# Optimization experiments

Measured on AMD Instinct MI355X. Metric: run time of the kernel, lower is better.

The kernel has to match this reference:

```python
import jax, jax.numpy as jnp
import numpy as np

NEG_BIG = -9e15

def setup_inputs() -> dict:
    key = jax.random.key(0)
    k1, k2, k3, k4 = jax.random.split(key, 4)
    N, Fin, Fout = 8192, 256, 128
    x = jax.random.normal(k1, (N, Fin), dtype=jnp.float32)
    adj = jax.random.randint(k2, (N, N), 0, 2, dtype=jnp.int32)
    # xavier-uniform-like init
    limW = float(np.sqrt(6.0 / (Fin + Fout)))
    W = jax.random.uniform(k3, (Fin, Fout), minval=-limW, maxval=limW, dtype=jnp.float32)
    lima = float(np.sqrt(6.0 / (2 * Fout + 1)))
    a = jax.random.uniform(k4, (2 * Fout, 1), minval=-lima, maxval=lima, dtype=jnp.float32)
    return {"x": x, "adj": adj, "W": W, "a": a}

def reference(x, adj, W, a, alpha=0.2):
    # h: (N, Fout)
    h = x @ W
    Fout = W.shape[1]
    # Split a into source/target halves: e[i,j] = leakyrelu(h_i·a1 + h_j·a2)
    a1, a2 = a[:Fout, 0], a[Fout:, 0]
    s = h @ a1  # (N,) row (source) scores
    t = h @ a2  # (N,) col (target) scores
    e = jax.nn.leaky_relu(s[:, None] + t[None, :], negative_slope=alpha)  # (N, N)
    e = jnp.where(adj > 0, e, NEG_BIG)
    attention = jax.nn.softmax(e, axis=1)
    # dropout omitted (eval mode / training=False)
    return attention @ h
```

## Files before the change

kernel.cpp:

```cpp
#include <hip/hip_runtime.h>
#include <hip/hip_bf16.h>

typedef __attribute__((ext_vector_type(8))) short short8;
typedef __attribute__((ext_vector_type(4))) short short4v;
typedef __attribute__((ext_vector_type(4))) float f32x4;

#define NR 8192
#define LOG2E 1.4426950408889634f

__device__ __forceinline__ short f2bf(float f) {
  return __builtin_bit_cast(short, __float2bfloat16(f));
}

__global__ __launch_bounds__(256) void k_pack(const int* __restrict__ adj,
                                              unsigned* __restrict__ mask) {
  size_t gid = (size_t)blockIdx.x * 256 + threadIdx.x;
  const int4* p = (const int4*)&adj[gid * 32];
  unsigned m = 0;
#pragma unroll
  for (int c = 0; c < 8; ++c) {
    int4 v = p[c];
    m |= (unsigned)(v.x > 0) << (c * 4 + 0);
    m |= (unsigned)(v.y > 0) << (c * 4 + 1);
    m |= (unsigned)(v.z > 0) << (c * 4 + 2);
    m |= (unsigned)(v.w > 0) << (c * 4 + 3);
  }
  mask[gid] = m;
}

__global__ __launch_bounds__(256) void k_gemm_h(const float* __restrict__ x,
                                                const float* __restrict__ W,
                                                const float* __restrict__ a,
                                                short* __restrict__ HT2,
                                                float* __restrict__ sv,
                                                float* __restrict__ tv) {
  __shared__ short WT[128][136];
  const int tid = threadIdx.x;
  const int w = tid >> 6;
  const int L = tid & 63;
  const int lm = L & 15;
  const int q = L >> 4;
  const int i0 = blockIdx.x * 64;

  f32x4 acc[8];
#pragma unroll
  for (int nn = 0; nn < 8; ++nn) acc[nn] = (f32x4){0.f, 0.f, 0.f, 0.f};

  for (int kc = 0; kc < 256; kc += 128) {
    if (kc) __syncthreads();
#pragma unroll
    for (int p = 0; p < 16; ++p) {
      int idx = p * 256 + tid;
      int k = idx >> 5;
      int f4 = (idx & 31) * 4;
      float4 v = *(const float4*)&W[(kc + k) * 128 + f4];
      WT[f4 + 0][k] = f2bf(v.x);
      WT[f4 + 1][k] = f2bf(v.y);
      WT[f4 + 2][k] = f2bf(v.z);
      WT[f4 + 3][k] = f2bf(v.w);
    }
    __syncthreads();
#pragma unroll
    for (int ks = 0; ks < 4; ++ks) {
      int row = i0 + 16 * w + lm;
      const float* xp = &x[(size_t)row * 256 + kc + ks * 32 + q * 8];
      float4 xa = *(const float4*)xp;
      float4 xb = *(const float4*)(xp + 4);
      short8 af;
      af[0] = f2bf(xa.x); af[1] = f2bf(xa.y); af[2] = f2bf(xa.z); af[3] = f2bf(xa.w);
      af[4] = f2bf(xb.x); af[5] = f2bf(xb.y); af[6] = f2bf(xb.z); af[7] = f2bf(xb.w);
#pragma unroll
      for (int nn = 0; nn < 8; ++nn) {
        short8 bf = *(const short8*)&WT[nn * 16 + lm][ks * 32 + q * 8];
        acc[nn] = __builtin_amdgcn_mfma_f32_16x16x32_bf16(af, bf, acc[nn], 0, 0, 0);
      }
    }
  }

  const int ib = i0 + 16 * w + 4 * q;
  const int tbase = (ib >> 5) * 4096 + (ib & 31);
  float a1v[8], a2v[8];
#pragma unroll
  for (int nn = 0; nn < 8; ++nn) {
    a1v[nn] = a[nn * 16 + lm];
    a2v[nn] = a[128 + nn * 16 + lm];
  }
  float sr[4] = {0.f, 0.f, 0.f, 0.f};
  float tr[4] = {0.f, 0.f, 0.f, 0.f};
#pragma unroll
  for (int nn = 0; nn < 8; ++nn) {
    int f = nn * 16 + lm;
    short4v o;
    o[0] = f2bf(acc[nn][0]);
    o[1] = f2bf(acc[nn][1]);
    o[2] = f2bf(acc[nn][2]);
    o[3] = f2bf(acc[nn][3]);
    *(short4v*)&HT2[tbase + f * 32] = o;
#pragma unroll
    for (int r = 0; r < 4; ++r) {
      sr[r] += acc[nn][r] * a1v[nn];
      tr[r] += acc[nn][r] * a2v[nn];
    }
  }
#pragma unroll
  for (int d = 1; d < 16; d <<= 1) {
#pragma unroll
    for (int r = 0; r < 4; ++r) {
      sr[r] += __shfl_xor(sr[r], d);
      tr[r] += __shfl_xor(tr[r], d);
    }
  }
  if (lm == 0) {
#pragma unroll
    for (int r = 0; r < 4; ++r) {
      sv[ib + r] = sr[r] * LOG2E;
      tv[ib + r] = tr[r] * LOG2E;
    }
  }
}

__global__ __launch_bounds__(64, 2) void k_flash(const unsigned* __restrict__ mask,
                                                 const short* __restrict__ HT2,
                                                 const float* __restrict__ sv,
                                                 const float* __restrict__ tv,
                                                 float* __restrict__ part,
                                                 float* __restrict__ lpart) {
  __shared__ float eps[32 * 128];
  const int L = threadIdx.x;
  const int lm = L & 15;
  const int q = L >> 4;
  const int sp = blockIdx.x & 7;
  const int it = blockIdx.x >> 3;
  const int i0 = it * 32;

  const int row0 = i0 + lm;
  const int row1 = row0 + 16;
  const float s0 = sv[row0];
  const float s1 = sv[row1];

  f32x4 acc[2][8];
#pragma unroll
  for (int mm = 0; mm < 2; ++mm)
#pragma unroll
    for (int nn = 0; nn < 8; ++nn) acc[mm][nn] = (f32x4){0.f, 0.f, 0.f, 0.f};
  float l0 = 0.f, l1 = 0.f;

  const int tile0 = sp * 32;
  const short* tp = &HT2[tile0 * 4096 + (lm * 32 + q * 8)];
  short8 sbf[8];
#pragma unroll
  for (int nn = 0; nn < 8; ++nn) sbf[nn] = *(const short8*)&tp[nn * 512];
  float4 stv0 = *(const float4*)&tv[tile0 * 32 + q * 8];
  float4 stv1 = *(const float4*)&tv[tile0 * 32 + q * 8 + 4];
  uint4 mg0 = *(const uint4*)&mask[row0 * 256 + tile0];
  uint4 mg1 = *(const uint4*)&mask[row1 * 256 + tile0];

  unsigned mwa0[4], mwa1[4];
#pragma unroll 4
  for (int t = 0; t < 32; ++t) {
    short8 bf[8];
#pragma unroll
    for (int nn = 0; nn < 8; ++nn) bf[nn] = sbf[nn];
    float4 tv0 = stv0, tv1 = stv1;
    if ((t & 3) == 0) {
      mwa0[0] = mg0.x; mwa0[1] = mg0.y; mwa0[2] = mg0.z; mwa0[3] = mg0.w;
      mwa1[0] = mg1.x; mwa1[1] = mg1.y; mwa1[2] = mg1.z; mwa1[3] = mg1.w;
      if (t + 4 < 32) {
        mg0 = *(const uint4*)&mask[row0 * 256 + tile0 + t + 4];
        mg1 = *(const uint4*)&mask[row1 * 256 + tile0 + t + 4];
      }
    }
    if (t + 1 < 32) {
      const short* np = &HT2[(tile0 + t + 1) * 4096 + (lm * 32 + q * 8)];
#pragma unroll
      for (int nn = 0; nn < 8; ++nn) sbf[nn] = *(const short8*)&np[nn * 512];
      stv0 = *(const float4*)&tv[(tile0 + t + 1) * 32 + q * 8];
      stv1 = *(const float4*)&tv[(tile0 + t + 1) * 32 + q * 8 + 4];
    }

    const unsigned b0 = (mwa0[t & 3] >> (q * 8)) & 0xffu;
    const unsigned b1 = (mwa1[t & 3] >> (q * 8)) & 0xffu;
    float tvl[8] = {tv0.x, tv0.y, tv0.z, tv0.w, tv1.x, tv1.y, tv1.z, tv1.w};
    short8 p0, p1;
#pragma unroll
    for (int e = 0; e < 8; ++e) {
      float v0 = s0 + tvl[e];
      float e0 = fmaxf(v0, 0.2f * v0);
      float pp0 = (b0 & (1u << e)) ? __builtin_amdgcn_exp2f(e0) : 0.f;
      l0 += pp0;
      p0[e] = f2bf(pp0);
      float v1 = s1 + tvl[e];
      float e1 = fmaxf(v1, 0.2f * v1);
      float pp1 = (b1 & (1u << e)) ? __builtin_amdgcn_exp2f(e1) : 0.f;
      l1 += pp1;
      p1[e] = f2bf(pp1);
    }
#pragma unroll
    for (int nn = 0; nn < 8; ++nn) {
      acc[0][nn] = __builtin_amdgcn_mfma_f32_16x16x32_bf16(p0, bf[nn], acc[0][nn], 0, 0, 0);
      acc[1][nn] = __builtin_amdgcn_mfma_f32_16x16x32_bf16(p1, bf[nn], acc[1][nn], 0, 0, 0);
    }
  }

#pragma unroll
  for (int mm = 0; mm < 2; ++mm)
#pragma unroll
    for (int nn = 0; nn < 8; ++nn)
#pragma unroll
      for (int r = 0; r < 4; ++r)
        eps[(16 * mm + 4 * q + r) * 128 + nn * 16 + lm] = acc[mm][nn][r];
  float* pbase = part + ((size_t)sp * NR + i0) * 128;
#pragma unroll
  for (int c = 0; c < 16; ++c) {
    int idx = (c * 64 + L) * 4;
    *(float4*)&pbase[idx] = *(const float4*)&eps[idx];
  }

  l0 += __shfl_xor(l0, 16);
  l0 += __shfl_xor(l0, 32);
  l1 += __shfl_xor(l1, 16);
  l1 += __shfl_xor(l1, 32);
  if (q == 0) {
    lpart[sp * NR + row0] = l0;
    lpart[sp * NR + row1] = l1;
  }
}

__global__ __launch_bounds__(256) void k_reduce(const float* __restrict__ part,
                                                const float* __restrict__ lpart,
                                                float* __restrict__ out, int S) {
  int idx4 = blockIdx.x * 256 + threadIdx.x;
  int idx = idx4 * 4;
  int i = idx >> 7;
  float4 sum = {0.f, 0.f, 0.f, 0.f};
  for (int sp = 0; sp < S; ++sp) {
    float4 v = *(const float4*)&part[(size_t)sp * (NR * 128) + idx];
    sum.x += v.x; sum.y += v.y; sum.z += v.z; sum.w += v.w;
  }
  float l = 0.f;
  for (int sp = 0; sp < S; ++sp) l += lpart[sp * NR + i];
  float inv = (l > 0.f) ? 1.f / l : 0.f;
  float4 o = {sum.x * inv, sum.y * inv, sum.z * inv, sum.w * inv};
  *(float4*)&out[idx] = o;
}

extern "C" void kernel_launch(void* const* d_in, const int* in_sizes, int n_in,
                              void* d_out, int out_size, void* d_ws, size_t ws_size,
                              hipStream_t stream) {
  const float* x = (const float*)d_in[0];
  const int* adj = (const int*)d_in[1];
  const float* W = (const float*)d_in[2];
  const float* a = (const float*)d_in[3];
  float* out = (float*)d_out;

  char* ws = (char*)d_ws;
  short* HT2 = (short*)(ws + 0);
  float* sv = (float*)(ws + 2097152);
  float* tv = (float*)(ws + 2129920);
  float* lpart = (float*)(ws + 2162688);
  unsigned* mask = (unsigned*)(ws + 2686976);
  float* part = (float*)(ws + 11599872);

  const int S = 8;

  hipLaunchKernelGGL(k_pack, dim3((NR * NR / 32) / 256), dim3(256), 0, stream, adj, mask);
  hipLaunchKernelGGL(k_gemm_h, dim3(128), dim3(256), 0, stream, x, W, a, HT2, sv, tv);
  hipLaunchKernelGGL(k_flash, dim3(256 * S), dim3(64), 0, stream, mask, HT2, sv, tv,
                     part, lpart);
  hipLaunchKernelGGL(k_reduce, dim3((NR * 128) / 1024), dim3(256), 0, stream, part,
                     lpart, out, S);
}
```

Baseline: 443.7 us.

## Fuse adjacency mask packing into flash kernel by reading adj directly

Removes the separate bit-packing kernel. The attention kernel now loads the int32 adjacency values directly, prefetching them one tile ahead, and tests each with `> 0`. This drops the 8 MB packed-mask write and read plus one launch. In exchange the flash kernel must stream the full 256 MB int adjacency itself with only 64-thread blocks, and it holds more prefetch registers, so it may become bandwidth- or latency-bound.

```diff
diff --git a/kernel.cpp b/kernel.cpp
--- a/kernel.cpp
+++ b/kernel.cpp
@@ -10,22 +10,6 @@
 
 __device__ __forceinline__ short f2bf(float f) {
   return __builtin_bit_cast(short, __float2bfloat16(f));
-}
-
-__global__ __launch_bounds__(256) void k_pack(const int* __restrict__ adj,
-                                              unsigned* __restrict__ mask) {
-  size_t gid = (size_t)blockIdx.x * 256 + threadIdx.x;
-  const int4* p = (const int4*)&adj[gid * 32];
-  unsigned m = 0;
-#pragma unroll
-  for (int c = 0; c < 8; ++c) {
-    int4 v = p[c];
-    m |= (unsigned)(v.x > 0) << (c * 4 + 0);
-    m |= (unsigned)(v.y > 0) << (c * 4 + 1);
-    m |= (unsigned)(v.z > 0) << (c * 4 + 2);
-    m |= (unsigned)(v.w > 0) << (c * 4 + 3);
-  }
-  mask[gid] = m;
 }
 
 __global__ __launch_bounds__(256) void k_gemm_h(const float* __restrict__ x,
@@ -119,7 +103,7 @@
   }
 }
 
-__global__ __launch_bounds__(64, 2) void k_flash(const unsigned* __restrict__ mask,
+__global__ __launch_bounds__(64, 2) void k_flash(const int* __restrict__ adj,
                                                  const short* __restrict__ HT2,
                                                  const float* __restrict__ sv,
                                                  const float* __restrict__ tv,
@@ -137,6 +121,8 @@
   const int row1 = row0 + 16;
   const float s0 = sv[row0];
   const float s1 = sv[row1];
+  const size_t ar0 = (size_t)row0 * NR;
+  const size_t ar1 = (size_t)row1 * NR;
 
   f32x4 acc[2][8];
 #pragma unroll
@@ -146,52 +132,52 @@
   float l0 = 0.f, l1 = 0.f;
 
   const int tile0 = sp * 32;
+  int jb = tile0 * 32 + q * 8;
+  int4 sa00 = *(const int4*)&adj[ar0 + jb];
+  int4 sa01 = *(const int4*)&adj[ar0 + jb + 4];
+  int4 sa10 = *(const int4*)&adj[ar1 + jb];
+  int4 sa11 = *(const int4*)&adj[ar1 + jb + 4];
   const short* tp = &HT2[tile0 * 4096 + (lm * 32 + q * 8)];
   short8 sbf[8];
 #pragma unroll
   for (int nn = 0; nn < 8; ++nn) sbf[nn] = *(const short8*)&tp[nn * 512];
-  float4 stv0 = *(const float4*)&tv[tile0 * 32 + q * 8];
-  float4 stv1 = *(const float4*)&tv[tile0 * 32 + q * 8 + 4];
-  uint4 mg0 = *(const uint4*)&mask[row0 * 256 + tile0];
-  uint4 mg1 = *(const uint4*)&mask[row1 * 256 + tile0];
-
-  unsigned mwa0[4], mwa1[4];
+  float4 stv0 = *(const float4*)&tv[jb];
+  float4 stv1 = *(const float4*)&tv[jb + 4];
+
 #pragma unroll 4
   for (int t = 0; t < 32; ++t) {
+    int4 a00 = sa00, a01 = sa01, a10 = sa10, a11 = sa11;
     short8 bf[8];
 #pragma unroll
     for (int nn = 0; nn < 8; ++nn) bf[nn] = sbf[nn];
     float4 tv0 = stv0, tv1 = stv1;
-    if ((t & 3) == 0) {
-      mwa0[0] = mg0.x; mwa0[1] = mg0.y; mwa0[2] = mg0.z; mwa0[3] = mg0.w;
-      mwa1[0] = mg1.x; mwa1[1] = mg1.y; mwa1[2] = mg1.z; mwa1[3] = mg1.w;
-      if (t + 4 < 32) {
-        mg0 = *(const uint4*)&mask[row0 * 256 + tile0 + t + 4];
-        mg1 = *(const uint4*)&mask[row1 * 256 + tile0 + t + 4];
-      }
-    }
     if (t + 1 < 32) {
+      int jn = (tile0 + t + 1) * 32 + q * 8;
+      sa00 = *(const int4*)&adj[ar0 + jn];
+      sa01 = *(const int4*)&adj[ar0 + jn + 4];
+      sa10 = *(const int4*)&adj[ar1 + jn];
+      sa11 = *(const int4*)&adj[ar1 + jn + 4];
       const short* np = &HT2[(tile0 + t + 1) * 4096 + (lm * 32 + q * 8)];
 #pragma unroll
       for (int nn = 0; nn < 8; ++nn) sbf[nn] = *(const short8*)&np[nn * 512];
-      stv0 = *(const float4*)&tv[(tile0 + t + 1) * 32 + q * 8];
-      stv1 = *(const float4*)&tv[(tile0 + t + 1) * 32 + q * 8 + 4];
-    }
-
-    const unsigned b0 = (mwa0[t & 3] >> (q * 8)) & 0xffu;
-    const unsigned b1 = (mwa1[t & 3] >> (q * 8)) & 0xffu;
+      stv0 = *(const float4*)&tv[jn];
+      stv1 = *(const float4*)&tv[jn + 4];
+    }
+
+    int av0[8] = {a00.x, a00.y, a00.z, a00.w, a01.x, a01.y, a01.z, a01.w};
+    int av1[8] = {a10.x, a10.y, a10.z, a10.w, a11.x, a11.y, a11.z, a11.w};
     float tvl[8] = {tv0.x, tv0.y, tv0.z, tv0.w, tv1.x, tv1.y, tv1.z, tv1.w};
     short8 p0, p1;
 #pragma unroll
     for (int e = 0; e < 8; ++e) {
       float v0 = s0 + tvl[e];
       float e0 = fmaxf(v0, 0.2f * v0);
-      float pp0 = (b0 & (1u << e)) ? __builtin_amdgcn_exp2f(e0) : 0.f;
+      float pp0 = (av0[e] > 0) ? __builtin_amdgcn_exp2f(e0) : 0.f;
       l0 += pp0;
       p0[e] = f2bf(pp0);
       float v1 = s1 + tvl[e];
       float e1 = fmaxf(v1, 0.2f * v1);
-      float pp1 = (b1 & (1u << e)) ? __builtin_amdgcn_exp2f(e1) : 0.f;
+      float pp1 = (av1[e] > 0) ? __builtin_amdgcn_exp2f(e1) : 0.f;
       l1 += pp1;
       p1[e] = f2bf(pp1);
     }
@@ -258,14 +244,12 @@
   float* sv = (float*)(ws + 2097152);
   float* tv = (float*)(ws + 2129920);
   float* lpart = (float*)(ws + 2162688);
-  unsigned* mask = (unsigned*)(ws + 2686976);
-  float* part = (float*)(ws + 11599872);
+  float* part = (float*)(ws + 2424832);
 
   const int S = 8;
 
-  hipLaunchKernelGGL(k_pack, dim3((NR * NR / 32) / 256), dim3(256), 0, stream, adj, mask);
   hipLaunchKernelGGL(k_gemm_h, dim3(128), dim3(256), 0, stream, x, W, a, HT2, sv, tv);
-  hipLaunchKernelGGL(k_flash, dim3(256 * S), dim3(64), 0, stream, mask, HT2, sv, tv,
+  hipLaunchKernelGGL(k_flash, dim3(256 * S), dim3(64), 0, stream, adj, HT2, sv, tv,
                      part, lpart);
   hipLaunchKernelGGL(k_reduce, dim3((NR * 128) / 1024), dim3(256), 0, stream, part,
                      lpart, out, S);
```

Measured after the change: 450.7 us. No clear change (+1.6%).
